# Optimization experiments

Hardware: AMD Instinct MI355X
Metric: run time of the kernel (lower is better)

## Reference

```python
import jax, jax.numpy as jnp
import numpy as np

EPS = 1e-6

def _rotate(z, q):
    # rotation trick (Householder-style reflection chain), z,q: [M, D]
    sg = jax.lax.stop_gradient
    z_norm = z / (jnp.linalg.norm(z, axis=1, keepdims=True) + EPS)
    q_norm = q / (jnp.linalg.norm(q, axis=1, keepdims=True) + EPS)
    w = sg((z_norm + q_norm) / jnp.linalg.norm(z_norm + q_norm, axis=1, keepdims=True))
    zn_d = sg(z_norm)
    qn_d = sg(q_norm)
    e = z - 2.0 * jnp.sum(z * w, axis=1, keepdims=True) * w \
          + 2.0 * jnp.sum(z * zn_d, axis=1, keepdims=True) * qn_d
    scale = sg(jnp.linalg.norm(q, axis=1, keepdims=True) / (jnp.linalg.norm(z, axis=1, keepdims=True) + EPS))
    return e * scale

def setup_inputs() -> dict:
    key = jax.random.key(0)
    k1, k2 = jax.random.split(key)
    x = jax.random.normal(k1, (16, 2048, 512), dtype=jnp.float32)
    codebooks = jax.random.normal(k2, (8, 1024, 512), dtype=jnp.float32)
    return {"x": x, "codebooks": codebooks}

def reference(x, codebooks):
    # x: [B, N, D]; codebooks: [Q, C, D]
    B, N, D = x.shape
    Q, C, _ = codebooks.shape
    sg = jax.lax.stop_gradient
    cb_sq = jnp.sum(codebooks * codebooks, axis=-1)  # [Q, C]
    residual = x
    quantized_out = jnp.zeros_like(x)
    all_indices = []
    all_losses = []
    for qi in range(Q):
        cb = codebooks[qi]                               # [C, D]
        flat = residual.reshape(-1, D)                   # [B*N, D]
        # squared euclidean distance: ||r||^2 - 2 r.c + ||c||^2
        d2 = jnp.sum(flat * flat, axis=1, keepdims=True) - 2.0 * (flat @ cb.T) + cb_sq[qi]
        ind = jnp.argmin(d2, axis=1)                     # [B*N]
        quant_raw = jnp.take(cb, ind, axis=0)            # [B*N, D]
        # commitment loss (codebook frozen per freeze_codebook=True)
        loss = jnp.mean((sg(quant_raw) - flat) ** 2)
        # rotation-trick transform of the quantized vectors
        quant = _rotate(flat, quant_raw).reshape(B, N, D)
        residual = residual - sg(quant)
        quantized_out = quantized_out + quant
        all_indices.append(ind.reshape(B, N))
        all_losses.append(loss)
    all_indices = jnp.stack(all_indices, axis=-1)        # [B, N, Q]
    all_losses = jnp.stack(all_losses, axis=-1)          # [Q]
    return quantized_out, all_indices, all_losses
```

## Files before the change

### kernel.cpp

```cpp
#include <hip/hip_runtime.h>

#define EPS 1e-6f

typedef __attribute__((ext_vector_type(8))) short bf16x8;
typedef __attribute__((ext_vector_type(4))) float f32x4;
typedef __attribute__((ext_vector_type(8))) unsigned short ushort8;

#define AS1(p) ((const __attribute__((address_space(1))) void*)(p))
#define AS3(p) ((__attribute__((address_space(3))) void*)(p))

__device__ inline unsigned int fkey(float f) {
  unsigned int u = __float_as_uint(f);
  return (u & 0x80000000u) ? ~u : (u | 0x80000000u);
}

__device__ inline unsigned long long shfl_xor_u64(unsigned long long v, int mask) {
  unsigned int lo = (unsigned int)(v & 0xffffffffull);
  unsigned int hi = (unsigned int)(v >> 32);
  lo = (unsigned int)__shfl_xor((int)lo, mask);
  hi = (unsigned int)__shfl_xor((int)hi, mask);
  return (((unsigned long long)hi) << 32) | lo;
}

__device__ inline unsigned short f2bf(float f) {
  unsigned int u = __float_as_uint(f);
  u += 0x7fffu + ((u >> 16) & 1u);
  return (unsigned short)(u >> 16);
}
__device__ inline float bf2f(unsigned short h) {
  return __uint_as_float(((unsigned int)h) << 16);
}

__device__ inline unsigned lds_off(const void* p) {
  return (unsigned)(unsigned long long)(__attribute__((address_space(3))) const void*)p;
}

template<int OFF>
__device__ inline bf16x8 ds_read128(unsigned addr) {
  bf16x8 r;
  asm volatile("ds_read_b128 %0, %1 offset:%2" : "=v"(r) : "v"(addr), "i"(OFF));
  return r;
}

template<int OFF>
__device__ inline float gload_f32(unsigned long long a) {
  float r;
  asm volatile("global_load_dword %0, %1, off offset:%2" : "=v"(r) : "v"(a), "i"(OFF));
  return r;
}

__global__ __launch_bounds__(256) void prep_kernel(
    const float* __restrict__ x, const float* __restrict__ cbs,
    unsigned short* __restrict__ Rhi, unsigned short* __restrict__ Rlo,
    unsigned short* __restrict__ CBhi, unsigned short* __restrict__ CBlo,
    float* __restrict__ cbsq, float* __restrict__ loss_out) {
  constexpr size_t M = 32768, D = 512, C = 1024, Q = 8;
  const size_t nthreads = (size_t)gridDim.x * 256;
  const size_t gtid = (size_t)blockIdx.x * 256 + threadIdx.x;
  const int lane = threadIdx.x & 63;
  const int w = threadIdx.x >> 6;

  for (size_t i = gtid; i < M * D / 8; i += nthreads) {
    size_t off = i * 8;
    float4 v0 = *(const float4*)(x + off);
    float4 v1 = *(const float4*)(x + off + 4);
    float v[8] = {v0.x, v0.y, v0.z, v0.w, v1.x, v1.y, v1.z, v1.w};
    ushort8 h, l;
    #pragma unroll
    for (int j = 0; j < 8; j++) {
      unsigned short hh = f2bf(v[j]);
      h[j] = hh;
      l[j] = f2bf(v[j] - bf2f(hh));
    }
    *(ushort8*)(Rhi + off) = h;
    *(ushort8*)(Rlo + off) = l;
  }
  for (size_t i = gtid; i < Q * C * D / 8; i += nthreads) {
    size_t off = i * 8;
    float4 v0 = *(const float4*)(cbs + off);
    float4 v1 = *(const float4*)(cbs + off + 4);
    float v[8] = {v0.x, v0.y, v0.z, v0.w, v1.x, v1.y, v1.z, v1.w};
    ushort8 h, l;
    #pragma unroll
    for (int j = 0; j < 8; j++) {
      unsigned short hh = f2bf(v[j]);
      h[j] = hh;
      l[j] = f2bf(v[j] - bf2f(hh));
    }
    *(ushort8*)(CBhi + off) = h;
    *(ushort8*)(CBlo + off) = l;
  }
  for (int row = blockIdx.x * 4 + w; row < (int)(Q * C); row += gridDim.x * 4) {
    const float4* p = (const float4*)(cbs + (size_t)row * 512);
    float4 v0 = p[lane];
    float4 v1 = p[lane + 64];
    float s = v0.x*v0.x + v0.y*v0.y + v0.z*v0.z + v0.w*v0.w
            + v1.x*v1.x + v1.y*v1.y + v1.z*v1.z + v1.w*v1.w;
    #pragma unroll
    for (int off = 32; off; off >>= 1) s += __shfl_xor(s, off);
    if (lane == 0) cbsq[row] = s;
  }
  if (blockIdx.x == 0 && threadIdx.x < (int)Q) loss_out[threadIdx.x] = 0.f;
}

__global__ __launch_bounds__(512, 2) void stage_kernel(
    const float* __restrict__ x, const float* __restrict__ cbq_f32,
    unsigned short* __restrict__ Rhi, unsigned short* __restrict__ Rlo,
    const unsigned short* __restrict__ Chi, const unsigned short* __restrict__ Clo,
    const float* __restrict__ cq_base, float* __restrict__ qout,
    float* __restrict__ idx_out, float* __restrict__ loss_out,
    int qi, int last) {
  __shared__ unsigned short As[3][2][128 * 32];
  __shared__ unsigned short Bs[3][2][256 * 32];
  __shared__ unsigned long long bestLDS[4][128];
  __shared__ float ls[8];

  const int tid = threadIdx.x;
  const int lane = tid & 63;
  const int w = tid >> 6;
  const int wr = w >> 2, wc = w & 3;
  const int row0 = blockIdx.x * 128;

  const int rw = lane >> 2, oq = lane & 3;
  const int o_sw = (oq - rw - (rw >> 2)) & 3;
  const int m = lane & 15, g = lane >> 4;
  const int f_sw8 = ((g + m + (m >> 2)) & 3) * 8;

  const unsigned short* pAhi = Rhi + (size_t)(row0 + w * 16 + rw) * 512 + o_sw * 8;
  const unsigned short* pAlo = Rlo + (size_t)(row0 + w * 16 + rw) * 512 + o_sw * 8;
  const unsigned short* pBhi = Chi + (size_t)(w * 32 + rw) * 512 + o_sw * 8;
  const unsigned short* pBlo = Clo + (size_t)(w * 32 + rw) * 512 + o_sw * 8;

  unsigned aA = lds_off(&As[0][0][(wr * 64 + m) * 32 + f_sw8]);
  unsigned aB = lds_off(&Bs[0][0][(wc * 64 + m) * 32 + f_sw8]);

  unsigned long long best[4][4];
  #pragma unroll
  for (int mi = 0; mi < 4; mi++)
    #pragma unroll
    for (int r = 0; r < 4; r++) best[mi][r] = ~0ull;

  auto stage = [&](int buf, int t) {
    const size_t ko = (size_t)((t & 15) * 32);
    const size_t cof = (size_t)((t >> 4) * 256) * 512;
    unsigned short* dAh = &As[buf][0][w * 512];
    unsigned short* dAl = &As[buf][1][w * 512];
    unsigned short* dBh = &Bs[buf][0][w * 1024];
    unsigned short* dBl = &Bs[buf][1][w * 1024];
    __builtin_amdgcn_global_load_lds(AS1(pAhi + ko), AS3(dAh), 16, 0, 0);
    __builtin_amdgcn_global_load_lds(AS1(pAlo + ko), AS3(dAl), 16, 0, 0);
    __builtin_amdgcn_global_load_lds(AS1(pBhi + cof + ko), AS3(dBh), 16, 0, 0);
    __builtin_amdgcn_global_load_lds(AS1(pBhi + cof + ko + 8192), AS3(dBh + 512), 16, 0, 0);
    __builtin_amdgcn_global_load_lds(AS1(pBlo + cof + ko), AS3(dBl), 16, 0, 0);
    __builtin_amdgcn_global_load_lds(AS1(pBlo + cof + ko + 8192), AS3(dBl + 512), 16, 0, 0);
  };

  float cq[4][4];
  {
    unsigned long long cqp = (unsigned long long)(cq_base + wc * 64 + m);
    cq[0][0] = gload_f32<0>(cqp);    cq[0][1] = gload_f32<64>(cqp);
    cq[0][2] = gload_f32<128>(cqp);  cq[0][3] = gload_f32<192>(cqp);
    cq[1][0] = gload_f32<1024>(cqp); cq[1][1] = gload_f32<1088>(cqp);
    cq[1][2] = gload_f32<1152>(cqp); cq[1][3] = gload_f32<1216>(cqp);
    cq[2][0] = gload_f32<2048>(cqp); cq[2][1] = gload_f32<2112>(cqp);
    cq[2][2] = gload_f32<2176>(cqp); cq[2][3] = gload_f32<2240>(cqp);
    cq[3][0] = gload_f32<3072>(cqp); cq[3][1] = gload_f32<3136>(cqp);
    cq[3][2] = gload_f32<3200>(cqp); cq[3][3] = gload_f32<3264>(cqp);
    asm volatile("s_waitcnt vmcnt(0)" ::: "memory");
  }

  bf16x8 f0_ah[4], f0_al[4], f0_bh[4], f0_bl[4];
  bf16x8 f1_ah[4], f1_al[4], f1_bh[4], f1_bl[4];
  f32x4 acc[4][4];
  int bn = 0;
  int bst = 2;

  stage(0, 0);
  asm volatile("s_waitcnt vmcnt(0)" ::: "memory");
  asm volatile("s_barrier" ::: "memory");
  __builtin_amdgcn_sched_barrier(0);

  f0_bh[0] = ds_read128<0>(aB);     f0_bh[1] = ds_read128<1024>(aB);
  f0_bh[2] = ds_read128<2048>(aB);  f0_bh[3] = ds_read128<3072>(aB);
  f0_bl[0] = ds_read128<16384>(aB); f0_bl[1] = ds_read128<17408>(aB);
  f0_bl[2] = ds_read128<18432>(aB); f0_bl[3] = ds_read128<19456>(aB);
  f0_ah[0] = ds_read128<0>(aA);     f0_ah[1] = ds_read128<1024>(aA);
  f0_ah[2] = ds_read128<2048>(aA);  f0_ah[3] = ds_read128<3072>(aA);
  f0_al[0] = ds_read128<8192>(aA);  f0_al[1] = ds_read128<9216>(aA);
  f0_al[2] = ds_read128<10240>(aA); f0_al[3] = ds_read128<11264>(aA);
  aA += 16384; aB += 32768; bn = 1;

  stage(1, 1);
  asm volatile("s_waitcnt lgkmcnt(0)" ::: "memory");
  asm volatile("s_waitcnt vmcnt(0)" ::: "memory");
  asm volatile("s_barrier" ::: "memory");
  __builtin_amdgcn_sched_barrier(0);

#define K_ITER(T, RD, CS)                                                        \
  {                                                                              \
    const int t_ = (T);                                                          \
    if (t_ < 63) {         \
      RD##_bh[0] = ds_read128<0>(aB);     RD##_bh[1] = ds_read128<1024>(aB);     \
      RD##_bh[2] = ds_read128<2048>(aB);  RD##_bh[3] = ds_read128<3072>(aB);     \
      RD##_bl[0] = ds_read128<16384>(aB); RD##_bl[1] = ds_read128<17408>(aB);    \
      RD##_bl[2] = ds_read128<18432>(aB); RD##_bl[3] = ds_read128<19456>(aB);    \
      RD##_ah[0] = ds_read128<0>(aA);     RD##_ah[1] = ds_read128<1024>(aA);     \
      RD##_ah[2] = ds_read128<2048>(aA);  RD##_ah[3] = ds_read128<3072>(aA);     \
      RD##_al[0] = ds_read128<8192>(aA);  RD##_al[1] = ds_read128<9216>(aA);     \
      RD##_al[2] = ds_read128<10240>(aA);                                        \
    }                                                                            \
    if (t_ < 62) { stage(bst, t_ + 2); bst = (bst == 2) ? 0 : bst + 1; }         \
                  \
    if (t_ < 63) asm volatile("s_waitcnt lgkmcnt(15)" ::: "memory");             \
    else         asm volatile("s_waitcnt lgkmcnt(0)" ::: "memory");              \
    __builtin_amdgcn_sched_barrier(0);                                           \
    if (t_ < 63) {                               \
      RD##_al[3] = ds_read128<11264>(aA);                                        \
      const int s_ = (bn == 2) ? -2 : 1;                                         \
      aA += s_ * 16384; aB += s_ * 32768; bn = (bn == 2) ? 0 : bn + 1;           \
    }                                                                            \
    if ((t_ & 15) == 0) {                                                        \
      _Pragma("unroll") for (int mi = 0; mi < 4; mi++)                           \
        _Pragma("unroll") for (int ni = 0; ni < 4; ni++)                         \
          acc[mi][ni] = (f32x4){0.f, 0.f, 0.f, 0.f};                             \
    }                                                                            \
    __builtin_amdgcn_s_setprio(1);                                               \
    _Pragma("unroll") for (int mi = 0; mi < 4; mi++)                             \
      _Pragma("unroll") for (int ni = 0; ni < 4; ni++)                           \
        acc[mi][ni] = __builtin_amdgcn_mfma_f32_16x16x32_bf16(                   \
            CS##_ah[mi], CS##_bh[ni], acc[mi][ni], 0, 0, 0);                     \
    _Pragma("unroll") for (int mi = 0; mi < 4; mi++)                             \
      _Pragma("unroll") for (int ni = 0; ni < 4; ni++)                           \
        acc[mi][ni] = __builtin_amdgcn_mfma_f32_16x16x32_bf16(                   \
            CS##_ah[mi], CS##_bl[ni], acc[mi][ni], 0, 0, 0);                     \
    _Pragma("unroll") for (int mi = 0; mi < 4; mi++)                             \
      _Pragma("unroll") for (int ni = 0; ni < 4; ni++)                           \
        acc[mi][ni] = __builtin_amdgcn_mfma_f32_16x16x32_bf16(                   \
            CS##_al[mi], CS##_bh[ni], acc[mi][ni], 0, 0, 0);                     \
    __builtin_amdgcn_s_setprio(0);                                               \
    if ((t_ & 15) == 15) {       \
      const int ct_ = t_ >> 4;                                                   \
      const unsigned colb = ct_ * 256 + wc * 64 + m;                             \
      _Pragma("unroll") for (int mi = 0; mi < 4; mi++)                           \
        _Pragma("unroll") for (int r = 0; r < 4; r++) {                          \
          _Pragma("unroll") for (int ni = 0; ni < 4; ni++) {                     \
            float d2 = fmaf(-2.f, acc[mi][ni][r], cq[ct_][ni]);                  \
            unsigned long long p =                                               \
                (((unsigned long long)fkey(d2)) << 32) | (colb + ni * 16);       \
            if (p < best[mi][r]) best[mi][r] = p;                                \
          }                                                                      \
        }                                                                        \
    }                                                                            \
    asm volatile("s_waitcnt vmcnt(0)" ::: "memory");   \
    asm volatile("s_barrier" ::: "memory");                                      \
    __builtin_amdgcn_sched_barrier(0);                                           \
  }

  for (int tp = 0; tp < 32; tp++) {
    K_ITER(tp * 2,     f1, f0);
    K_ITER(tp * 2 + 1, f0, f1);
  }
#undef K_ITER

  #pragma unroll
  for (int mi = 0; mi < 4; mi++)
    #pragma unroll
    for (int r = 0; r < 4; r++) {
      unsigned long long mn = best[mi][r];
      #pragma unroll
      for (int off = 1; off < 16; off <<= 1) {
        unsigned long long o = shfl_xor_u64(mn, off);
        if (o < mn) mn = o;
      }
      best[mi][r] = mn;
    }

  if (m == 0) {
    #pragma unroll
    for (int mi = 0; mi < 4; mi++)
      #pragma unroll
      for (int r = 0; r < 4; r++)
        bestLDS[wc][wr * 64 + mi * 16 + g * 4 + r] = best[mi][r];
  }
  __syncthreads();

  float lossacc = 0.f;
  for (int rr = 0; rr < 16; rr++) {
    const int row128 = w * 16 + rr;
    unsigned long long mn = bestLDS[0][row128];
    #pragma unroll
    for (int q2 = 1; q2 < 4; q2++) {
      unsigned long long o = bestLDS[q2][row128];
      if (o < mn) mn = o;
    }
    const int c = (int)(mn & 0xffffffffu);
    const int row = row0 + row128;
    if (lane == 0) idx_out[(size_t)row * 8 + qi] = (float)c;

    const size_t base = (size_t)row * 512 + lane * 8;
    ushort8 h = *(const ushort8*)(Rhi + base);
    ushort8 l = *(const ushort8*)(Rlo + base);
    const float* qrow = cbq_f32 + (size_t)c * 512 + lane * 8;
    float4 q0 = *(const float4*)qrow;
    float4 q1 = *(const float4*)(qrow + 4);
    float z[8], q[8] = {q0.x, q0.y, q0.z, q0.w, q1.x, q1.y, q1.z, q1.w};
    #pragma unroll
    for (int j = 0; j < 8; j++) z[j] = bf2f(h[j]) + bf2f(l[j]);

    float zz = 0.f, qq = 0.f, zq = 0.f;
    #pragma unroll
    for (int j = 0; j < 8; j++) {
      zz = fmaf(z[j], z[j], zz);
      qq = fmaf(q[j], q[j], qq);
      zq = fmaf(z[j], q[j], zq);
    }
    #pragma unroll
    for (int off = 32; off; off >>= 1) {
      zz += __shfl_xor(zz, off);
      qq += __shfl_xor(qq, off);
      zq += __shfl_xor(zq, off);
    }

    float nz = sqrtf(zz), nq = sqrtf(qq);
    float inz = 1.f / (nz + EPS), inq = 1.f / (nq + EPS);
    float ns  = sqrtf(zz*inz*inz + 2.f*zq*inz*inq + qq*inq*inq);
    float ins = 1.f / ns;
    float zw  = (zz*inz + zq*inq) * ins;
    float zzn = zz * inz;
    float scale = nq * inz;
    float az = scale * (1.f - 2.f * zw * ins * inz);
    float aq = scale * (2.f * zzn - 2.f * zw * ins) * inq;

    if (!last) {
      #pragma unroll
      for (int j = 0; j < 8; j++) {
        float r = z[j] - (az * z[j] + aq * q[j]);
        unsigned short hh = f2bf(r);
        h[j] = hh;
        l[j] = f2bf(r - bf2f(hh));
      }
      *(ushort8*)(Rhi + base) = h;
      *(ushort8*)(Rlo + base) = l;
    } else {
      float4 x0 = *(const float4*)(x + base);
      float4 x1 = *(const float4*)(x + base + 4);
      float xv[8] = {x0.x, x0.y, x0.z, x0.w, x1.x, x1.y, x1.z, x1.w};
      float o[8];
      #pragma unroll
      for (int j = 0; j < 8; j++) {
        float r = z[j] - (az * z[j] + aq * q[j]);
        o[j] = xv[j] - r;
      }
      *(float4*)(qout + base)     = (float4){o[0], o[1], o[2], o[3]};
      *(float4*)(qout + base + 4) = (float4){o[4], o[5], o[6], o[7]};
    }
    lossacc += (zz - 2.f * zq + qq);
  }
  if (lane == 0) ls[w] = lossacc;
  __syncthreads();
  if (tid == 0)
    atomicAdd(loss_out + qi, (ls[0] + ls[1] + ls[2] + ls[3] +
                              ls[4] + ls[5] + ls[6] + ls[7]) *
                             (1.f / (32768.f * 512.f)));
}

extern "C" void kernel_launch(void* const* d_in, const int* in_sizes, int n_in,
                              void* d_out, int out_size, void* d_ws, size_t ws_size,
                              hipStream_t stream) {
  const float* x   = (const float*)d_in[0];
  const float* cbs = (const float*)d_in[1];
  float* out = (float*)d_out;
  const size_t M = 32768, D = 512, Q = 8, C = 1024;
  float* qout     = out;
  float* idx_out  = out + M * D;
  float* loss_out = idx_out + M * Q;

  unsigned short* Rhi  = (unsigned short*)d_ws;
  unsigned short* Rlo  = Rhi + M * D;
  unsigned short* CBhi = Rlo + M * D;
  unsigned short* CBlo = CBhi + Q * C * D;
  float* cbsq = (float*)(CBlo + Q * C * D);

  prep_kernel<<<512, 256, 0, stream>>>(x, cbs, Rhi, Rlo, CBhi, CBlo, cbsq, loss_out);

  for (int qi = 0; qi < (int)Q; qi++) {
    stage_kernel<<<256, 512, 0, stream>>>(
        x, cbs + (size_t)qi * C * D, Rhi, Rlo,
        CBhi + (size_t)qi * C * D, CBlo + (size_t)qi * C * D,
        cbsq + qi * C, qout, idx_out, loss_out, qi, qi == (int)Q - 1 ? 1 : 0);
  }
}
```

Before: 1.163 ms.

## Shrink stage-kernel row tile to 64 with 4 waves and double-buffered LDS

Result: slower. 1.517 ms (+30.4%).

```diff
diff --git a/kernel.cpp b/kernel.cpp
--- a/kernel.cpp
+++ b/kernel.cpp
@@ -103,23 +103,20 @@
   if (blockIdx.x == 0 && threadIdx.x < (int)Q) loss_out[threadIdx.x] = 0.f;
 }
 
-__global__ __launch_bounds__(512, 2) void stage_kernel(
+__global__ __launch_bounds__(256, 2) void stage_kernel(
     const float* __restrict__ x, const float* __restrict__ cbq_f32,
     unsigned short* __restrict__ Rhi, unsigned short* __restrict__ Rlo,
     const unsigned short* __restrict__ Chi, const unsigned short* __restrict__ Clo,
     const float* __restrict__ cq_base, float* __restrict__ qout,
     float* __restrict__ idx_out, float* __restrict__ loss_out,
     int qi, int last) {
-  __shared__ unsigned short As[3][2][128 * 32];
-  __shared__ unsigned short Bs[3][2][256 * 32];
-  __shared__ unsigned long long bestLDS[4][128];
-  __shared__ float ls[8];
+  __shared__ unsigned short SM[40960];
 
   const int tid = threadIdx.x;
   const int lane = tid & 63;
   const int w = tid >> 6;
-  const int wr = w >> 2, wc = w & 3;
-  const int row0 = blockIdx.x * 128;
+  const int wc = w;
+  const int row0 = blockIdx.x * 64;
 
   const int rw = lane >> 2, oq = lane & 3;
   const int o_sw = (oq - rw - (rw >> 2)) & 3;
@@ -128,11 +125,11 @@
 
   const unsigned short* pAhi = Rhi + (size_t)(row0 + w * 16 + rw) * 512 + o_sw * 8;
   const unsigned short* pAlo = Rlo + (size_t)(row0 + w * 16 + rw) * 512 + o_sw * 8;
-  const unsigned short* pBhi = Chi + (size_t)(w * 32 + rw) * 512 + o_sw * 8;
-  const unsigned short* pBlo = Clo + (size_t)(w * 32 + rw) * 512 + o_sw * 8;
-
-  unsigned aA = lds_off(&As[0][0][(wr * 64 + m) * 32 + f_sw8]);
-  unsigned aB = lds_off(&Bs[0][0][(wc * 64 + m) * 32 + f_sw8]);
+  const unsigned short* pBhi = Chi + (size_t)(w * 64 + rw) * 512 + o_sw * 8;
+  const unsigned short* pBlo = Clo + (size_t)(w * 64 + rw) * 512 + o_sw * 8;
+
+  const unsigned aA = lds_off(&SM[m * 32 + f_sw8]);
+  const unsigned aB = lds_off(&SM[8192 + (wc * 64 + m) * 32 + f_sw8]);
 
   unsigned long long best[4][4];
   #pragma unroll
@@ -143,16 +140,19 @@
   auto stage = [&](int buf, int t) {
     const size_t ko = (size_t)((t & 15) * 32);
     const size_t cof = (size_t)((t >> 4) * 256) * 512;
-    unsigned short* dAh = &As[buf][0][w * 512];
-    unsigned short* dAl = &As[buf][1][w * 512];
-    unsigned short* dBh = &Bs[buf][0][w * 1024];
-    unsigned short* dBl = &Bs[buf][1][w * 1024];
+    unsigned short* dAh = &SM[buf * 4096 + w * 512];
+    unsigned short* dAl = dAh + 2048;
+    unsigned short* dBh = &SM[8192 + buf * 16384 + w * 2048];
+    unsigned short* dBl = dBh + 8192;
     __builtin_amdgcn_global_load_lds(AS1(pAhi + ko), AS3(dAh), 16, 0, 0);
     __builtin_amdgcn_global_load_lds(AS1(pAlo + ko), AS3(dAl), 16, 0, 0);
-    __builtin_amdgcn_global_load_lds(AS1(pBhi + cof + ko), AS3(dBh), 16, 0, 0);
-    __builtin_amdgcn_global_load_lds(AS1(pBhi + cof + ko + 8192), AS3(dBh + 512), 16, 0, 0);
-    __builtin_amdgcn_global_load_lds(AS1(pBlo + cof + ko), AS3(dBl), 16, 0, 0);
-    __builtin_amdgcn_global_load_lds(AS1(pBlo + cof + ko + 8192), AS3(dBl + 512), 16, 0, 0);
+    #pragma unroll
+    for (int cc = 0; cc < 4; cc++) {
+      __builtin_amdgcn_global_load_lds(AS1(pBhi + cof + ko + cc * 8192),
+                                       AS3(dBh + cc * 512), 16, 0, 0);
+      __builtin_amdgcn_global_load_lds(AS1(pBlo + cof + ko + cc * 8192),
+                                       AS3(dBl + cc * 512), 16, 0, 0);
+    }
   };
 
   float cq[4][4];
@@ -172,8 +172,6 @@
   bf16x8 f0_ah[4], f0_al[4], f0_bh[4], f0_bl[4];
   bf16x8 f1_ah[4], f1_al[4], f1_bh[4], f1_bl[4];
   f32x4 acc[4][4];
-  int bn = 0;
-  int bst = 2;
 
   stage(0, 0);
   asm volatile("s_waitcnt vmcnt(0)" ::: "memory");
@@ -186,9 +184,8 @@
   f0_bl[2] = ds_read128<18432>(aB); f0_bl[3] = ds_read128<19456>(aB);
   f0_ah[0] = ds_read128<0>(aA);     f0_ah[1] = ds_read128<1024>(aA);
   f0_ah[2] = ds_read128<2048>(aA);  f0_ah[3] = ds_read128<3072>(aA);
-  f0_al[0] = ds_read128<8192>(aA);  f0_al[1] = ds_read128<9216>(aA);
-  f0_al[2] = ds_read128<10240>(aA); f0_al[3] = ds_read128<11264>(aA);
-  aA += 16384; aB += 32768; bn = 1;
+  f0_al[0] = ds_read128<4096>(aA);  f0_al[1] = ds_read128<5120>(aA);
+  f0_al[2] = ds_read128<6144>(aA);  f0_al[3] = ds_read128<7168>(aA);
 
   stage(1, 1);
   asm volatile("s_waitcnt lgkmcnt(0)" ::: "memory");
@@ -196,29 +193,35 @@
   asm volatile("s_barrier" ::: "memory");
   __builtin_amdgcn_sched_barrier(0);
 
-#define K_ITER(T, RD, CS)                                                        \
+#define K_ITER(T, RD, CS, BS, SB)                                                \
   {                                                                              \
     const int t_ = (T);                                                          \
-    if (t_ < 63) {         \
-      RD##_bh[0] = ds_read128<0>(aB);     RD##_bh[1] = ds_read128<1024>(aB);     \
-      RD##_bh[2] = ds_read128<2048>(aB);  RD##_bh[3] = ds_read128<3072>(aB);     \
-      RD##_bl[0] = ds_read128<16384>(aB); RD##_bl[1] = ds_read128<17408>(aB);    \
-      RD##_bl[2] = ds_read128<18432>(aB); RD##_bl[3] = ds_read128<19456>(aB);    \
-      RD##_ah[0] = ds_read128<0>(aA);     RD##_ah[1] = ds_read128<1024>(aA);     \
-      RD##_ah[2] = ds_read128<2048>(aA);  RD##_ah[3] = ds_read128<3072>(aA);     \
-      RD##_al[0] = ds_read128<8192>(aA);  RD##_al[1] = ds_read128<9216>(aA);     \
-      RD##_al[2] = ds_read128<10240>(aA);                                        \
+    if (t_ < 63) {               \
+      RD##_bh[0] = ds_read128<(BS)*32768 + 0>(aB);                               \
+      RD##_bh[1] = ds_read128<(BS)*32768 + 1024>(aB);                            \
+      RD##_bh[2] = ds_read128<(BS)*32768 + 2048>(aB);                            \
+      RD##_bh[3] = ds_read128<(BS)*32768 + 3072>(aB);                            \
+      RD##_bl[0] = ds_read128<(BS)*32768 + 16384>(aB);                           \
+      RD##_bl[1] = ds_read128<(BS)*32768 + 17408>(aB);                           \
+      RD##_bl[2] = ds_read128<(BS)*32768 + 18432>(aB);                           \
+      RD##_bl[3] = ds_read128<(BS)*32768 + 19456>(aB);                           \
+      RD##_ah[0] = ds_read128<(BS)*8192 + 0>(aA);                                \
+      RD##_ah[1] = ds_read128<(BS)*8192 + 1024>(aA);                             \
+      RD##_ah[2] = ds_read128<(BS)*8192 + 2048>(aA);                             \
+      RD##_ah[3] = ds_read128<(BS)*8192 + 3072>(aA);                             \
+      RD##_al[0] = ds_read128<(BS)*8192 + 4096>(aA);                             \
+      RD##_al[1] = ds_read128<(BS)*8192 + 5120>(aA);                             \
+      RD##_al[2] = ds_read128<(BS)*8192 + 6144>(aA);                             \
+                   \
+      asm volatile("s_waitcnt lgkmcnt(15)" ::: "memory");                        \
+    } else {                                                                     \
+      asm volatile("s_waitcnt lgkmcnt(0)" ::: "memory");                         \
     }                                                                            \
-    if (t_ < 62) { stage(bst, t_ + 2); bst = (bst == 2) ? 0 : bst + 1; }         \
-                  \
-    if (t_ < 63) asm volatile("s_waitcnt lgkmcnt(15)" ::: "memory");             \
-    else         asm volatile("s_waitcnt lgkmcnt(0)" ::: "memory");              \
     __builtin_amdgcn_sched_barrier(0);                                           \
-    if (t_ < 63) {                               \
-      RD##_al[3] = ds_read128<11264>(aA);                                        \
-      const int s_ = (bn == 2) ? -2 : 1;                                         \
-      aA += s_ * 16384; aB += s_ * 32768; bn = (bn == 2) ? 0 : bn + 1;           \
-    }                                                                            \
+    asm volatile("s_barrier" ::: "memory");  \
+    if (t_ < 63) RD##_al[3] = ds_read128<(BS)*8192 + 7168>(aA);                  \
+    if (t_ < 62) stage(SB, t_ + 2);           \
+    __builtin_amdgcn_sched_barrier(0);                                           \
     if ((t_ & 15) == 0) {                                                        \
       _Pragma("unroll") for (int mi = 0; mi < 4; mi++)                           \
         _Pragma("unroll") for (int ni = 0; ni < 4; ni++)                         \
@@ -251,14 +254,14 @@
           }                                                                      \
         }                                                                        \
     }                                                                            \
-    asm volatile("s_waitcnt vmcnt(0)" ::: "memory");   \
-    asm volatile("s_barrier" ::: "memory");                                      \
+    asm volatile("s_waitcnt vmcnt(0)" ::: "memory");  \
+    asm volatile("s_barrier" ::: "memory");             \
     __builtin_amdgcn_sched_barrier(0);                                           \
   }
 
   for (int tp = 0; tp < 32; tp++) {
-    K_ITER(tp * 2,     f1, f0);
-    K_ITER(tp * 2 + 1, f0, f1);
+    K_ITER(tp * 2,     f1, f0, 1, 0);
+    K_ITER(tp * 2 + 1, f0, f1, 0, 1);
   }
 #undef K_ITER
 
@@ -275,26 +278,30 @@
       best[mi][r] = mn;
     }
 
+  unsigned long long* bestLDS = (unsigned long long*)&SM[0];
+  float* ls = (float*)(bestLDS + 256);
+  __syncthreads();
+
   if (m == 0) {
     #pragma unroll
     for (int mi = 0; mi < 4; mi++)
       #pragma unroll
       for (int r = 0; r < 4; r++)
-        bestLDS[wc][wr * 64 + mi * 16 + g * 4 + r] = best[mi][r];
+        bestLDS[wc * 64 + mi * 16 + g * 4 + r] = best[mi][r];
   }
   __syncthreads();
 
   float lossacc = 0.f;
   for (int rr = 0; rr < 16; rr++) {
-    const int row128 = w * 16 + rr;
-    unsigned long long mn = bestLDS[0][row128];
+    const int row64 = w * 16 + rr;
+    unsigned long long mn = bestLDS[row64];
     #pragma unroll
     for (int q2 = 1; q2 < 4; q2++) {
-      unsigned long long o = bestLDS[q2][row128];
+      unsigned long long o = bestLDS[q2 * 64 + row64];
       if (o < mn) mn = o;
     }
     const int c = (int)(mn & 0xffffffffu);
-    const int row = row0 + row128;
+    const int row = row0 + row64;
     if (lane == 0) idx_out[(size_t)row * 8 + qi] = (float)c;
 
     const size_t base = (size_t)row * 512 + lane * 8;
@@ -359,8 +366,7 @@
   if (lane == 0) ls[w] = lossacc;
   __syncthreads();
   if (tid == 0)
-    atomicAdd(loss_out + qi, (ls[0] + ls[1] + ls[2] + ls[3] +
-                              ls[4] + ls[5] + ls[6] + ls[7]) *
+    atomicAdd(loss_out + qi, (ls[0] + ls[1] + ls[2] + ls[3]) *
                              (1.f / (32768.f * 512.f)));
 }
 
@@ -384,7 +390,7 @@
   prep_kernel<<<512, 256, 0, stream>>>(x, cbs, Rhi, Rlo, CBhi, CBlo, cbsq, loss_out);
 
   for (int qi = 0; qi < (int)Q; qi++) {
-    stage_kernel<<<256, 512, 0, stream>>>(
+    stage_kernel<<<512, 256, 0, stream>>>(
         x, cbs + (size_t)qi * C * D, Rhi, Rlo,
         CBhi + (size_t)qi * C * D, CBlo + (size_t)qi * C * D,
         cbsq + qi * C, qout, idx_out, loss_out, qi, qi == (int)Q - 1 ? 1 : 0);
```
